# Optimization experiments

Hardware: AMD Instinct MI355X
Metric: run time of the kernel (lower is better)

Reference implementation:

```python
import jax, jax.numpy as jnp
import numpy as np

B, S, H, I, E, K = 2, 512, 512, 1024, 64, 4


def setup_inputs() -> dict:
    key = jax.random.key(0)
    ks = jax.random.split(key, 16)
    scale = jnp.float32(0.02)

    def w(k, shape):
        return jax.random.normal(k, shape, dtype=jnp.float32) * scale

    return {
        "x": jax.random.normal(ks[0], (B, S, H), dtype=jnp.float32),
        "router_w": w(ks[1], (E, H)),
        "router_b": w(ks[2], (E,)),
        "expert_biases": jnp.zeros((E,), dtype=jnp.float32),
        "sw1": w(ks[3], (I, H)), "sb1": w(ks[4], (I,)),
        "sw2": w(ks[5], (H, I)), "sb2": w(ks[6], (H,)),
        "sw3": w(ks[7], (I, H)), "sb3": w(ks[8], (I,)),
        "w1": w(ks[9], (E, I, H)), "b1": w(ks[10], (E, I)),
        "w2": w(ks[11], (E, H, I)), "b2": w(ks[12], (E, H)),
        "w3": w(ks[13], (E, I, H)), "b3": w(ks[14], (E, I)),
        "top_k": K,
    }


def _ffn(x, w1, b1, w2, b2, w3, b3):
    return (jax.nn.silu(x @ w1.T + b1) * (x @ w3.T + b3)) @ w2.T + b2


def reference(x, router_w, router_b, expert_biases,
              sw1, sb1, sw2, sb2, sw3, sb3,
              w1, b1, w2, b2, w3, b3, top_k):
    Bx, Sx, Hx = x.shape
    Ex = router_w.shape[0]

    # Router: logits [B,S,E]; top-k selection uses bias-adjusted logits,
    # but gates come from the ORIGINAL (unbiased) logits.
    logits = x @ router_w.T + router_b
    _, idx = jax.lax.top_k(logits + expert_biases, top_k)  # [B,S,K] int32
    orig = jnp.take_along_axis(logits, idx, axis=-1)       # [B,S,K]
    scores = jax.nn.sigmoid(orig)
    gates = scores / jnp.maximum(jnp.sum(scores, axis=-1, keepdims=True), 1e-12)

    # Shared expert(s): num_shared_experts == 1, divided by 1.
    shared = _ffn(x, sw1, sb1, sw2, sb2, sw3, sb3)

    # Combine gates into a dense per-token per-expert gate matrix [T,E].
    xf = x.reshape(-1, Hx)                 # [T,H]
    T = xf.shape[0]
    tok = jnp.arange(T)[:, None]
    gate_full = jnp.zeros((T, Ex), x.dtype).at[tok, idx.reshape(T, top_k)].add(
        gates.reshape(T, top_k))

    # Routed experts: each expert FFN over all tokens, gated combine.
    # (Mathematically identical to the original masked-dense loop: the mask
    #  zeroes both inputs and gates of unassigned tokens.)
    def body(acc, p):
        ew1, eb1, ew2, eb2, ew3, eb3, g = p
        y = _ffn(xf, ew1, eb1, ew2, eb2, ew3, eb3)  # [T,H]
        return acc + g[:, None] * y, None

    acc, _ = jax.lax.scan(body, jnp.zeros_like(xf),
                          (w1, b1, w2, b2, w3, b3, gate_full.T))

    return shared + acc.reshape(x.shape)
```

## Files before the change

### kernel.cpp

```cpp
#include <hip/hip_runtime.h>
#include <math.h>

#define T_    1024
#define H_    512
#define I_    1024
#define E_    64
#define K_    4
#define NPAIR (T_*K_)
#define NENT  (NPAIR + T_)

#define BM 128
#define BN 64
#define BKS 64
#define LDP 72
#define MAXWORK 160

typedef float  f32x4  __attribute__((ext_vector_type(4)));
typedef short  bf16x8 __attribute__((ext_vector_type(8)));

__device__ __forceinline__ ushort f2bf(float f) {
    uint u = __float_as_uint(f);
    u += 0x7fffu + ((u >> 16) & 1u);
    return (ushort)(u >> 16);
}

__global__ __launch_bounds__(64) void moe_router(
    const float* __restrict__ x, const float* __restrict__ rw,
    const float* __restrict__ rb, const float* __restrict__ eb,
    int* __restrict__ idx_out, float* __restrict__ gate_out)
{
    const int t = blockIdx.x;
    const int lane = threadIdx.x;
    __shared__ float xs[H_];
    __shared__ float lg[E_];
    __shared__ float bs[E_];
    for (int i = lane; i < H_; i += 64) xs[i] = x[(size_t)t*H_ + i];
    bs[lane] = eb[lane];
    __syncthreads();
    float acc = 0.f;
    const float* wrow = rw + (size_t)lane*H_;
    for (int k = 0; k < H_; k += 4) {
        float4 w4 = *reinterpret_cast<const float4*>(wrow + k);
        acc = fmaf(xs[k+0], w4.x, acc);
        acc = fmaf(xs[k+1], w4.y, acc);
        acc = fmaf(xs[k+2], w4.z, acc);
        acc = fmaf(xs[k+3], w4.w, acc);
    }
    lg[lane] = acc + rb[lane];
    __syncthreads();
    if (lane == 0) {
        unsigned long long used = 0ull;
        int sel[K_]; float orig[K_];
        for (int k = 0; k < K_; ++k) {
            float best = -INFINITY; int bi = 0;
            for (int e = 0; e < E_; ++e) {
                if (used & (1ull << e)) continue;
                float v = lg[e] + bs[e];
                if (v > best) { best = v; bi = e; }
            }
            used |= (1ull << bi);
            sel[k] = bi; orig[k] = lg[bi];
        }
        float s[K_]; float sum = 0.f;
        for (int k = 0; k < K_; ++k) { s[k] = 1.f/(1.f + __expf(-orig[k])); sum += s[k]; }
        sum = fmaxf(sum, 1e-12f);
        for (int k = 0; k < K_; ++k) {
            idx_out[t*K_ + k] = sel[k];
            gate_out[t*K_ + k] = s[k] / sum;
        }
    }
}

__global__ __launch_bounds__(256) void moe_build(
    const int* __restrict__ idx, const float* __restrict__ gates,
    int* __restrict__ cnts, int* __restrict__ offs,
    int* __restrict__ entry_token, float* __restrict__ entry_gate,
    int* __restrict__ pair_pos,
    int* __restrict__ blk_e, int* __restrict__ blk_ro, int* __restrict__ nwork)
{
    __shared__ int c[E_];
    __shared__ int run[E_];
    const int tid = threadIdx.x;
    if (tid < E_) c[tid] = 0;
    __syncthreads();
    for (int p = tid; p < NPAIR; p += 256) atomicAdd(&c[idx[p]], 1);
    __syncthreads();
    if (tid == 0) {
        int o = 0;
        for (int e = 0; e < E_; ++e) { run[e] = o; offs[e] = o; cnts[e] = c[e]; o += c[e]; }
        offs[E_] = NPAIR;
        cnts[E_] = T_;
        int nb = 0;
        for (int e = 0; e <= E_; ++e) {
            int n = (e < E_) ? c[e] : T_;
            for (int ro = 0; ro < n; ro += BM) { blk_e[nb] = e; blk_ro[nb] = ro; ++nb; }
        }
        nwork[0] = nb;
    }
    __syncthreads();
    for (int p = tid; p < NPAIR; p += 256) {
        int e = idx[p];
        int pos = atomicAdd(&run[e], 1);
        entry_token[pos] = p / K_;
        entry_gate[pos]  = gates[p];
        pair_pos[p]      = pos;
    }
    for (int t = tid; t < T_; t += 256) {
        entry_token[NPAIR + t] = t;
        entry_gate[NPAIR + t]  = 1.0f;
    }
}

__global__ __launch_bounds__(512, 4) void moe_stage1(
    const float* __restrict__ x,
    const float* __restrict__ w1, const float* __restrict__ b1,
    const float* __restrict__ w3, const float* __restrict__ b3,
    const float* __restrict__ sw1, const float* __restrict__ sb1,
    const float* __restrict__ sw3, const float* __restrict__ sb3,
    const int* __restrict__ cnts, const int* __restrict__ offs,
    const int* __restrict__ entry_token,
    const int* __restrict__ blk_e, const int* __restrict__ blk_ro,
    const int* __restrict__ nwork,
    ushort* __restrict__ h1buf)
{
    const int w = blockIdx.x;
    if (w >= nwork[0]) return;
    const int e  = blk_e[w];
    const int ro = blk_ro[w];
    const int itile = blockIdx.y;
    const int n = cnts[e];
    const int off = offs[e];
    const int rows = min(BM, n - ro);
    const float* W1 = (e < E_) ? (w1 + (size_t)e*I_*H_) : sw1;
    const float* W3 = (e < E_) ? (w3 + (size_t)e*I_*H_) : sw3;
    const float* B1 = (e < E_) ? (b1 + (size_t)e*I_) : sb1;
    const float* B3 = (e < E_) ? (b3 + (size_t)e*I_) : sb3;

    __shared__ ushort Xs [BM][LDP];
    __shared__ ushort W1s[BN][LDP];
    __shared__ ushort W3s[BN][LDP];

    const int tid  = threadIdx.x;
    const int lane = tid & 63;
    const int wid  = tid >> 6;
    const int wm   = wid >> 1;
    const int wn   = wid & 1;
    const int l15  = lane & 15;
    const int lg   = lane >> 4;

    const int sr = tid >> 4;
    const int sc = tid & 15;

    const float* xp[4];
    const float* wp[2];
    #pragma unroll
    for (int i = 0; i < 4; ++i)
        xp[i] = x + (size_t)entry_token[off + ro + sr + i*32]*H_ + sc*4;
    #pragma unroll
    for (int i = 0; i < 2; ++i)
        wp[i] = W1 + (size_t)(itile*BN + sr + i*32)*H_ + sc*4;
    const ptrdiff_t d31 = (const float*)W3 - (const float*)W1;

    f32x4 acc1[2][2] = {};
    f32x4 acc3[2][2] = {};

    float4 xv[4], av[2], cv[2];
    #pragma unroll
    for (int i = 0; i < 4; ++i) xv[i] = *reinterpret_cast<const float4*>(xp[i]);
    #pragma unroll
    for (int i = 0; i < 2; ++i) {
        av[i] = *reinterpret_cast<const float4*>(wp[i]);
        cv[i] = *reinterpret_cast<const float4*>(wp[i] + d31);
    }

    for (int kc = 0; kc < H_; kc += BKS) {
        __syncthreads();
        #pragma unroll
        for (int i = 0; i < 4; ++i)
            *reinterpret_cast<ushort4*>(&Xs[sr + i*32][sc*4]) =
                make_ushort4(f2bf(xv[i].x), f2bf(xv[i].y), f2bf(xv[i].z), f2bf(xv[i].w));
        #pragma unroll
        for (int i = 0; i < 2; ++i) {
            *reinterpret_cast<ushort4*>(&W1s[sr + i*32][sc*4]) =
                make_ushort4(f2bf(av[i].x), f2bf(av[i].y), f2bf(av[i].z), f2bf(av[i].w));
            *reinterpret_cast<ushort4*>(&W3s[sr + i*32][sc*4]) =
                make_ushort4(f2bf(cv[i].x), f2bf(cv[i].y), f2bf(cv[i].z), f2bf(cv[i].w));
        }
        if (kc + BKS < H_) {
            const int kn = kc + BKS;
            #pragma unroll
            for (int i = 0; i < 4; ++i)
                xv[i] = *reinterpret_cast<const float4*>(xp[i] + kn);
            #pragma unroll
            for (int i = 0; i < 2; ++i) {
                av[i] = *reinterpret_cast<const float4*>(wp[i] + kn);
                cv[i] = *reinterpret_cast<const float4*>(wp[i] + kn + d31);
            }
        }
        __syncthreads();
        #pragma unroll
        for (int s = 0; s < 2; ++s) {
            bf16x8 a[2], bb1[2], bb3[2];
            #pragma unroll
            for (int f = 0; f < 2; ++f) {
                a[f]   = *reinterpret_cast<const bf16x8*>(&Xs [wm*32 + f*16 + l15][s*32 + lg*8]);
                bb1[f] = *reinterpret_cast<const bf16x8*>(&W1s[wn*32 + f*16 + l15][s*32 + lg*8]);
                bb3[f] = *reinterpret_cast<const bf16x8*>(&W3s[wn*32 + f*16 + l15][s*32 + lg*8]);
            }
            #pragma unroll
            for (int fm = 0; fm < 2; ++fm) {
                #pragma unroll
                for (int fn = 0; fn < 2; ++fn) {
                    acc1[fm][fn] = __builtin_amdgcn_mfma_f32_16x16x32_bf16(a[fm], bb1[fn], acc1[fm][fn], 0, 0, 0);
                    acc3[fm][fn] = __builtin_amdgcn_mfma_f32_16x16x32_bf16(a[fm], bb3[fn], acc3[fm][fn], 0, 0, 0);
                }
            }
        }
    }
    #pragma unroll
    for (int fm = 0; fm < 2; ++fm) {
        #pragma unroll
        for (int fn = 0; fn < 2; ++fn) {
            const int col = itile*BN + wn*32 + fn*16 + l15;
            const float bv1 = B1[col];
            const float bv3 = B3[col];
            #pragma unroll
            for (int j = 0; j < 4; ++j) {
                const int rl = wm*32 + fm*16 + lg*4 + j;
                if (rl < rows) {
                    float z1 = acc1[fm][fn][j] + bv1;
                    float z3 = acc3[fm][fn][j] + bv3;
                    float h = z1 / (1.f + __expf(-z1)) * z3;
                    h1buf[(size_t)(off+ro+rl)*I_ + col] = f2bf(h);
                }
            }
        }
    }
}

__global__ __launch_bounds__(512, 4) void moe_stage2(
    const ushort* __restrict__ h1buf,
    const float* __restrict__ w2, const float* __restrict__ b2,
    const float* __restrict__ sw2, const float* __restrict__ sb2,
    const int* __restrict__ cnts, const int* __restrict__ offs,
    const float* __restrict__ entry_gate,
    const int* __restrict__ blk_e, const int* __restrict__ blk_ro,
    const int* __restrict__ nwork,
    float* __restrict__ ybuf)
{
    const int w = blockIdx.x;
    if (w >= nwork[0]) return;
    const int e  = blk_e[w];
    const int ro = blk_ro[w];
    const int htile = blockIdx.y;
    const int n = cnts[e];
    const int off = offs[e];
    const int rows = min(BM, n - ro);
    const float* W2 = (e < E_) ? (w2 + (size_t)e*H_*I_) : sw2;
    const float* B2 = (e < E_) ? (b2 + (size_t)e*H_) : sb2;

    __shared__ ushort Hs[BM][LDP];
    __shared__ ushort Ws[BN][LDP];

    const int tid  = threadIdx.x;
    const int lane = tid & 63;
    const int wid  = tid >> 6;
    const int wm   = wid >> 1;
    const int wn   = wid & 1;
    const int l15  = lane & 15;
    const int lg   = lane >> 4;

    const int sr = tid >> 4;
    const int sc = tid & 15;
    const int hr = tid >> 3;
    const int hc = tid & 7;

    const ushort* hp[2];
    const float*  wp[2];
    #pragma unroll
    for (int i = 0; i < 2; ++i)
        hp[i] = h1buf + (size_t)(off + ro + hr + i*64)*I_ + hc*8;
    #pragma unroll
    for (int i = 0; i < 2; ++i)
        wp[i] = W2 + (size_t)(htile*BN + sr + i*32)*I_ + sc*4;

    f32x4 acc[2][2] = {};

    uint4  hv[2];
    float4 wv[2];
    #pragma unroll
    for (int i = 0; i < 2; ++i) hv[i] = *reinterpret_cast<const uint4*>(hp[i]);
    #pragma unroll
    for (int i = 0; i < 2; ++i) wv[i] = *reinterpret_cast<const float4*>(wp[i]);

    for (int kc = 0; kc < I_; kc += BKS) {
        __syncthreads();
        #pragma unroll
        for (int i = 0; i < 2; ++i)
            *reinterpret_cast<uint4*>(&Hs[hr + i*64][hc*8]) = hv[i];
        #pragma unroll
        for (int i = 0; i < 2; ++i)
            *reinterpret_cast<ushort4*>(&Ws[sr + i*32][sc*4]) =
                make_ushort4(f2bf(wv[i].x), f2bf(wv[i].y), f2bf(wv[i].z), f2bf(wv[i].w));
        if (kc + BKS < I_) {
            const int kn = kc + BKS;
            #pragma unroll
            for (int i = 0; i < 2; ++i)
                hv[i] = *reinterpret_cast<const uint4*>(hp[i] + kn);
            #pragma unroll
            for (int i = 0; i < 2; ++i)
                wv[i] = *reinterpret_cast<const float4*>(wp[i] + kn);
        }
        __syncthreads();
        #pragma unroll
        for (int s = 0; s < 2; ++s) {
            bf16x8 a[2], b[2];
            #pragma unroll
            for (int f = 0; f < 2; ++f) {
                a[f] = *reinterpret_cast<const bf16x8*>(&Hs[wm*32 + f*16 + l15][s*32 + lg*8]);
                b[f] = *reinterpret_cast<const bf16x8*>(&Ws[wn*32 + f*16 + l15][s*32 + lg*8]);
            }
            #pragma unroll
            for (int fm = 0; fm < 2; ++fm) {
                #pragma unroll
                for (int fn = 0; fn < 2; ++fn) {
                    acc[fm][fn] = __builtin_amdgcn_mfma_f32_16x16x32_bf16(a[fm], b[fn], acc[fm][fn], 0, 0, 0);
                }
            }
        }
    }
    #pragma unroll
    for (int fm = 0; fm < 2; ++fm) {
        #pragma unroll
        for (int fn = 0; fn < 2; ++fn) {
            const int col = htile*BN + wn*32 + fn*16 + l15;
            const float bv = B2[col];
            #pragma unroll
            for (int j = 0; j < 4; ++j) {
                const int rl = wm*32 + fm*16 + lg*4 + j;
                if (rl < rows) {
                    const float g = entry_gate[off + ro + rl];
                    ybuf[(size_t)(off+ro+rl)*H_ + col] = (acc[fm][fn][j] + bv) * g;
                }
            }
        }
    }
}

__global__ __launch_bounds__(128) void moe_combine(
    const float* __restrict__ ybuf, const int* __restrict__ pair_pos,
    float* __restrict__ out)
{
    const int t = blockIdx.x;
    const int lane = threadIdx.x;
    const int h = lane * 4;
    const int p0 = pair_pos[t*K_+0], p1 = pair_pos[t*K_+1];
    const int p2 = pair_pos[t*K_+2], p3 = pair_pos[t*K_+3];
    float4 a  = *reinterpret_cast<const float4*>(ybuf + (size_t)(NPAIR+t)*H_ + h);
    float4 v0 = *reinterpret_cast<const float4*>(ybuf + (size_t)p0*H_ + h);
    float4 v1 = *reinterpret_cast<const float4*>(ybuf + (size_t)p1*H_ + h);
    float4 v2 = *reinterpret_cast<const float4*>(ybuf + (size_t)p2*H_ + h);
    float4 v3 = *reinterpret_cast<const float4*>(ybuf + (size_t)p3*H_ + h);
    float4 r;
    r.x = a.x + v0.x + v1.x + v2.x + v3.x;
    r.y = a.y + v0.y + v1.y + v2.y + v3.y;
    r.z = a.z + v0.z + v1.z + v2.z + v3.z;
    r.w = a.w + v0.w + v1.w + v2.w + v3.w;
    *reinterpret_cast<float4*>(out + (size_t)t*H_ + h) = r;
}

extern "C" void kernel_launch(void* const* d_in, const int* in_sizes, int n_in,
                              void* d_out, int out_size, void* d_ws, size_t ws_size,
                              hipStream_t stream)
{
    const float* x   = (const float*)d_in[0];
    const float* rw  = (const float*)d_in[1];
    const float* rb  = (const float*)d_in[2];
    const float* eb  = (const float*)d_in[3];
    const float* sw1 = (const float*)d_in[4];
    const float* sb1 = (const float*)d_in[5];
    const float* sw2 = (const float*)d_in[6];
    const float* sb2 = (const float*)d_in[7];
    const float* sw3 = (const float*)d_in[8];
    const float* sb3 = (const float*)d_in[9];
    const float* w1  = (const float*)d_in[10];
    const float* b1  = (const float*)d_in[11];
    const float* w2  = (const float*)d_in[12];
    const float* b2  = (const float*)d_in[13];
    const float* w3  = (const float*)d_in[14];
    const float* b3  = (const float*)d_in[15];
    float* out = (float*)d_out;

    char* p = (char*)d_ws;
    auto take = [&](size_t bytes) { char* q = p; p += (bytes + 255) & ~(size_t)255; return q; };
    int*    idxb  = (int*)   take((size_t)NPAIR*4);
    float*  gateb = (float*) take((size_t)NPAIR*4);
    int*    cnts  = (int*)   take((E_+1)*4);
    int*    offs  = (int*)   take((E_+1)*4);
    int*    etok  = (int*)   take((size_t)NENT*4);
    float*  egate = (float*) take((size_t)NENT*4);
    int*    ppos  = (int*)   take((size_t)NPAIR*4);
    int*    blk_e = (int*)   take((size_t)MAXWORK*4);
    int*    blk_ro= (int*)   take((size_t)MAXWORK*4);
    int*    nwork = (int*)   take(4);
    ushort* h1buf = (ushort*)take((size_t)NENT*I_*2);
    float*  ybuf  = (float*) take((size_t)NENT*H_*4);

    moe_router <<<T_, 64, 0, stream>>>(x, rw, rb, eb, idxb, gateb);
    moe_build  <<<1, 256, 0, stream>>>(idxb, gateb, cnts, offs, etok, egate, ppos,
                                       blk_e, blk_ro, nwork);
    moe_stage1 <<<dim3(MAXWORK, I_/BN), 512, 0, stream>>>(x, w1, b1, w3, b3,
                                                          sw1, sb1, sw3, sb3,
                                                          cnts, offs, etok,
                                                          blk_e, blk_ro, nwork, h1buf);
    moe_stage2 <<<dim3(MAXWORK, H_/BN), 512, 0, stream>>>(h1buf, w2, b2, sw2, sb2,
                                                          cnts, offs, egate,
                                                          blk_e, blk_ro, nwork, ybuf);
    moe_combine<<<T_, 128, 0, stream>>>(ybuf, ppos, out);
}
```

Baseline: 235.7 us.

## Double-buffer LDS tiles and prefetch two stages ahead in expert GEMM kernels

Both expert GEMM kernels (gate/up and down projection) now use two LDS buffers and two register staging sets, so global loads run two K-tiles ahead. The LDS write for the next tile overlaps the MFMA work on the current one, needing one barrier per tile instead of two. Barriers use a custom s_waitcnt lgkmcnt(0) plus s_barrier rather than __syncthreads. The cost is double the LDS footprint and more live registers, which may lower occupancy.

```diff
diff --git a/kernel.cpp b/kernel.cpp
--- a/kernel.cpp
+++ b/kernel.cpp
@@ -14,14 +14,21 @@
 #define BKS 64
 #define LDP 72
 #define MAXWORK 160
+#define NT1 (H_/BKS)
+#define NT2 (I_/BKS)
 
 typedef float  f32x4  __attribute__((ext_vector_type(4)));
 typedef short  bf16x8 __attribute__((ext_vector_type(8)));
+
+#define BARRIER() asm volatile("s_waitcnt lgkmcnt(0)\n\ts_barrier" ::: "memory")
 
 __device__ __forceinline__ ushort f2bf(float f) {
     uint u = __float_as_uint(f);
     u += 0x7fffu + ((u >> 16) & 1u);
     return (ushort)(u >> 16);
+}
+__device__ __forceinline__ ushort4 cvt4(float4 v) {
+    return make_ushort4(f2bf(v.x), f2bf(v.y), f2bf(v.z), f2bf(v.w));
 }
 
 __global__ __launch_bounds__(64) void moe_router(
@@ -136,9 +143,9 @@
     const float* B1 = (e < E_) ? (b1 + (size_t)e*I_) : sb1;
     const float* B3 = (e < E_) ? (b3 + (size_t)e*I_) : sb3;
 
-    __shared__ ushort Xs [BM][LDP];
-    __shared__ ushort W1s[BN][LDP];
-    __shared__ ushort W3s[BN][LDP];
+    __shared__ ushort Xs [2][BM][LDP];
+    __shared__ ushort W1s[2][BN][LDP];
+    __shared__ ushort W3s[2][BN][LDP];
 
     const int tid  = threadIdx.x;
     const int lane = tid & 63;
@@ -152,10 +159,10 @@
     const int sc = tid & 15;
 
     const float* xp[4];
-    const float* wp[2];
     #pragma unroll
     for (int i = 0; i < 4; ++i)
         xp[i] = x + (size_t)entry_token[off + ro + sr + i*32]*H_ + sc*4;
+    const float* wp[2];
     #pragma unroll
     for (int i = 0; i < 2; ++i)
         wp[i] = W1 + (size_t)(itile*BN + sr + i*32)*H_ + sc*4;
@@ -164,48 +171,36 @@
     f32x4 acc1[2][2] = {};
     f32x4 acc3[2][2] = {};
 
-    float4 xv[4], av[2], cv[2];
-    #pragma unroll
-    for (int i = 0; i < 4; ++i) xv[i] = *reinterpret_cast<const float4*>(xp[i]);
-    #pragma unroll
-    for (int i = 0; i < 2; ++i) {
-        av[i] = *reinterpret_cast<const float4*>(wp[i]);
-        cv[i] = *reinterpret_cast<const float4*>(wp[i] + d31);
-    }
-
-    for (int kc = 0; kc < H_; kc += BKS) {
-        __syncthreads();
+    float4 A[8], B[8];
+
+    auto issue = [&](float4* R, int kc) {
+        #pragma unroll
+        for (int i = 0; i < 4; ++i) R[i] = *reinterpret_cast<const float4*>(xp[i] + kc);
+        #pragma unroll
+        for (int i = 0; i < 2; ++i) {
+            R[4+i] = *reinterpret_cast<const float4*>(wp[i] + kc);
+            R[6+i] = *reinterpret_cast<const float4*>(wp[i] + kc + d31);
+        }
+    };
+    auto cvtwrite = [&](const float4* R, int b) {
         #pragma unroll
         for (int i = 0; i < 4; ++i)
-            *reinterpret_cast<ushort4*>(&Xs[sr + i*32][sc*4]) =
-                make_ushort4(f2bf(xv[i].x), f2bf(xv[i].y), f2bf(xv[i].z), f2bf(xv[i].w));
+            *reinterpret_cast<ushort4*>(&Xs[b][sr + i*32][sc*4]) = cvt4(R[i]);
         #pragma unroll
         for (int i = 0; i < 2; ++i) {
-            *reinterpret_cast<ushort4*>(&W1s[sr + i*32][sc*4]) =
-                make_ushort4(f2bf(av[i].x), f2bf(av[i].y), f2bf(av[i].z), f2bf(av[i].w));
-            *reinterpret_cast<ushort4*>(&W3s[sr + i*32][sc*4]) =
-                make_ushort4(f2bf(cv[i].x), f2bf(cv[i].y), f2bf(cv[i].z), f2bf(cv[i].w));
-        }
-        if (kc + BKS < H_) {
-            const int kn = kc + BKS;
-            #pragma unroll
-            for (int i = 0; i < 4; ++i)
-                xv[i] = *reinterpret_cast<const float4*>(xp[i] + kn);
-            #pragma unroll
-            for (int i = 0; i < 2; ++i) {
-                av[i] = *reinterpret_cast<const float4*>(wp[i] + kn);
-                cv[i] = *reinterpret_cast<const float4*>(wp[i] + kn + d31);
-            }
-        }
-        __syncthreads();
+            *reinterpret_cast<ushort4*>(&W1s[b][sr + i*32][sc*4]) = cvt4(R[4+i]);
+            *reinterpret_cast<ushort4*>(&W3s[b][sr + i*32][sc*4]) = cvt4(R[6+i]);
+        }
+    };
+    auto mfma_step = [&](int b) {
         #pragma unroll
         for (int s = 0; s < 2; ++s) {
             bf16x8 a[2], bb1[2], bb3[2];
             #pragma unroll
             for (int f = 0; f < 2; ++f) {
-                a[f]   = *reinterpret_cast<const bf16x8*>(&Xs [wm*32 + f*16 + l15][s*32 + lg*8]);
-                bb1[f] = *reinterpret_cast<const bf16x8*>(&W1s[wn*32 + f*16 + l15][s*32 + lg*8]);
-                bb3[f] = *reinterpret_cast<const bf16x8*>(&W3s[wn*32 + f*16 + l15][s*32 + lg*8]);
+                a[f]   = *reinterpret_cast<const bf16x8*>(&Xs [b][wm*32 + f*16 + l15][s*32 + lg*8]);
+                bb1[f] = *reinterpret_cast<const bf16x8*>(&W1s[b][wn*32 + f*16 + l15][s*32 + lg*8]);
+                bb3[f] = *reinterpret_cast<const bf16x8*>(&W3s[b][wn*32 + f*16 + l15][s*32 + lg*8]);
             }
             #pragma unroll
             for (int fm = 0; fm < 2; ++fm) {
@@ -216,7 +211,25 @@
                 }
             }
         }
-    }
+    };
+
+    issue(A, 0);
+    issue(B, BKS);
+    cvtwrite(A, 0);
+    BARRIER();
+
+    #pragma unroll
+    for (int tt = 0; tt < NT1; tt += 2) {
+        mfma_step(0);
+        if (tt + 2 < NT1) issue(A, (tt + 2)*BKS);
+        cvtwrite(B, 1);
+        BARRIER();
+        mfma_step(1);
+        if (tt + 3 < NT1) issue(B, (tt + 3)*BKS);
+        if (tt + 2 < NT1) cvtwrite(A, 0);
+        BARRIER();
+    }
+
     #pragma unroll
     for (int fm = 0; fm < 2; ++fm) {
         #pragma unroll
@@ -259,8 +272,8 @@
     const float* W2 = (e < E_) ? (w2 + (size_t)e*H_*I_) : sw2;
     const float* B2 = (e < E_) ? (b2 + (size_t)e*H_) : sb2;
 
-    __shared__ ushort Hs[BM][LDP];
-    __shared__ ushort Ws[BN][LDP];
+    __shared__ ushort Hs[2][BM][LDP];
+    __shared__ ushort Ws[2][BN][LDP];
 
     const int tid  = threadIdx.x;
     const int lane = tid & 63;
@@ -276,59 +289,69 @@
     const int hc = tid & 7;
 
     const ushort* hp[2];
-    const float*  wp[2];
     #pragma unroll
     for (int i = 0; i < 2; ++i)
         hp[i] = h1buf + (size_t)(off + ro + hr + i*64)*I_ + hc*8;
+    const float* wp[2];
     #pragma unroll
     for (int i = 0; i < 2; ++i)
         wp[i] = W2 + (size_t)(htile*BN + sr + i*32)*I_ + sc*4;
 
     f32x4 acc[2][2] = {};
 
-    uint4  hv[2];
-    float4 wv[2];
-    #pragma unroll
-    for (int i = 0; i < 2; ++i) hv[i] = *reinterpret_cast<const uint4*>(hp[i]);
-    #pragma unroll
-    for (int i = 0; i < 2; ++i) wv[i] = *reinterpret_cast<const float4*>(wp[i]);
-
-    for (int kc = 0; kc < I_; kc += BKS) {
-        __syncthreads();
-        #pragma unroll
-        for (int i = 0; i < 2; ++i)
-            *reinterpret_cast<uint4*>(&Hs[hr + i*64][hc*8]) = hv[i];
-        #pragma unroll
-        for (int i = 0; i < 2; ++i)
-            *reinterpret_cast<ushort4*>(&Ws[sr + i*32][sc*4]) =
-                make_ushort4(f2bf(wv[i].x), f2bf(wv[i].y), f2bf(wv[i].z), f2bf(wv[i].w));
-        if (kc + BKS < I_) {
-            const int kn = kc + BKS;
-            #pragma unroll
-            for (int i = 0; i < 2; ++i)
-                hv[i] = *reinterpret_cast<const uint4*>(hp[i] + kn);
-            #pragma unroll
-            for (int i = 0; i < 2; ++i)
-                wv[i] = *reinterpret_cast<const float4*>(wp[i] + kn);
-        }
-        __syncthreads();
+    uint4  HA[2], HB[2];
+    float4 WA[2], WB[2];
+
+    auto issue = [&](uint4* HR, float4* WR, int kc) {
+        #pragma unroll
+        for (int i = 0; i < 2; ++i) {
+            HR[i] = *reinterpret_cast<const uint4*>(hp[i] + kc);
+            WR[i] = *reinterpret_cast<const float4*>(wp[i] + kc);
+        }
+    };
+    auto stwrite = [&](const uint4* HR, const float4* WR, int b) {
+        #pragma unroll
+        for (int i = 0; i < 2; ++i) {
+            *reinterpret_cast<uint4*>(&Hs[b][hr + i*64][hc*8]) = HR[i];
+            *reinterpret_cast<ushort4*>(&Ws[b][sr + i*32][sc*4]) = cvt4(WR[i]);
+        }
+    };
+    auto mfma_step = [&](int b) {
         #pragma unroll
         for (int s = 0; s < 2; ++s) {
-            bf16x8 a[2], b[2];
+            bf16x8 a[2], bb[2];
             #pragma unroll
             for (int f = 0; f < 2; ++f) {
-                a[f] = *reinterpret_cast<const bf16x8*>(&Hs[wm*32 + f*16 + l15][s*32 + lg*8]);
-                b[f] = *reinterpret_cast<const bf16x8*>(&Ws[wn*32 + f*16 + l15][s*32 + lg*8]);
+                a[f]  = *reinterpret_cast<const bf16x8*>(&Hs[b][wm*32 + f*16 + l15][s*32 + lg*8]);
+                bb[f] = *reinterpret_cast<const bf16x8*>(&Ws[b][wn*32 + f*16 + l15][s*32 + lg*8]);
             }
             #pragma unroll
             for (int fm = 0; fm < 2; ++fm) {
                 #pragma unroll
                 for (int fn = 0; fn < 2; ++fn) {
-                    acc[fm][fn] = __builtin_amdgcn_mfma_f32_16x16x32_bf16(a[fm], b[fn], acc[fm][fn], 0, 0, 0);
+                    acc[fm][fn] = __builtin_amdgcn_mfma_f32_16x16x32_bf16(a[fm], bb[fn], acc[fm][fn], 0, 0, 0);
                 }
             }
         }
-    }
+    };
+
+    issue(HA, WA, 0);
+    issue(HB, WB, BKS);
+    stwrite(HA, WA, 0);
+    BARRIER();
+
+    #pragma unroll
+    for (int tt = 0; tt < NT2; tt += 2) {
+        mfma_step(0);
+        if (tt + 2 < NT2) issue(HA, WA, (tt + 2)*BKS);
+        stwrite(HB, WB, 1);
+        BARRIER();
+        mfma_step(1);
+        if (tt + 3 < NT2) issue(HB, WB, (tt + 3)*BKS);
+        if (tt + 2 < NT2) stwrite(HA, WA, 0);
+        BARRIER();
+    }
+
     #pragma unroll
     for (int fm = 0; fm < 2; ++fm) {
         #pragma unroll
```

After: 232.2 us. About the same (-1.5%).
